# Optimization experiments

Hardware: AMD Instinct MI355X
Metric: run time of the kernel (lower is better)

The kernel has to match this reference:

```python
import jax, jax.numpy as jnp
import numpy as np

B, T, D = 4, 4096, 1024
EPS = 1e-6


def setup_inputs() -> dict:
    key = jax.random.key(0)
    ks = jax.random.split(key, 9)
    s = 0.02  # init scale for weights
    f32 = jnp.float32
    return {
        "x_seq": jax.random.normal(ks[0], (B, T, D), f32),
        "W_q": jax.random.normal(ks[1], (D, D), f32) * s,
        "b_q": jax.random.normal(ks[2], (D,), f32) * s,
        "W_k": jax.random.normal(ks[3], (D, D), f32) * s,
        "b_k": jax.random.normal(ks[4], (D,), f32) * s,
        "W_v": jax.random.normal(ks[5], (D, D), f32) * s,
        "b_v": jax.random.normal(ks[6], (D,), f32) * s,
        "W_a": jax.random.normal(ks[7], (D, D), f32) * s,
        "b_a": jax.random.normal(ks[8], (D,), f32) * s,
    }


def reference(x_seq, W_q, b_q, W_k, b_k, W_v, b_v, W_a, b_a):
    # torch nn.Linear: y = x @ W.T + b
    q = jax.nn.relu(x_seq @ W_q.T + b_q)          # [B,T,D]
    k = jax.nn.relu(x_seq @ W_k.T + b_k)          # [B,T,D]
    v = x_seq @ W_v.T + b_v                        # [B,T,D]
    A = jax.nn.sigmoid(x_seq @ W_a.T + b_a)       # [B,T,D]

    # cumprod_A[b,s,i] = prod_{u>=s} A[b,u,i], via reverse cumsum of logs
    log_g = jax.lax.cumsum(jnp.log(A + 1e-6), axis=1, reverse=True)
    wk = k * jnp.exp(log_g)                        # weighted_k [B,T,D]

    # num[b,t,j] = q_t . S_t[:,j] with S_t = cumsum_{s<=t} (wk_s outer v_s)
    # == causal-masked (q @ wk^T) @ v  (same math, no [B,T,D,D] blowup)
    scores = jnp.einsum('btd,bsd->bts', q, wk)     # [B,T,T]
    Tn = x_seq.shape[1]
    mask = jnp.tril(jnp.ones((Tn, Tn), bool))
    scores = jnp.where(mask, scores, 0.0)

    num = jnp.einsum('bts,bsd->btd', scores, v)    # [B,T,D]
    denom = scores.sum(-1, keepdims=True) + EPS    # q_t . Z_t, [B,T,1]
    return num / denom
```

## Files before the change

kernel.cpp:

```cpp
#include <hip/hip_runtime.h>

typedef unsigned short u16;
typedef unsigned int u32;

typedef __bf16 bf16x8 __attribute__((ext_vector_type(8)));
typedef float f32x4 __attribute__((ext_vector_type(4)));
typedef u16 u16x8 __attribute__((ext_vector_type(8)));

#define TSEQ 4096
#define DDIM 1024
#define NB 4
#define EPSV 1e-6f
#define CPITCH 136

__device__ __forceinline__ u16 f2b(float f) {
    union { float f; u32 u; } v; v.f = f;
    u32 r = v.u + 0x7FFFu + ((v.u >> 16) & 1u);
    return (u16)(r >> 16);
}
__device__ __forceinline__ float b2f(u16 h) {
    union { u32 u; float f; } v; v.u = ((u32)h) << 16; return v.f;
}
__device__ __forceinline__ u16 f2h(float f) {
    union { _Float16 h; u16 u; } v; v.h = (_Float16)f; return v.u;
}
__device__ __forceinline__ float h2f(u16 u) {
    union { u16 u; _Float16 h; } v; v.u = u; return (float)v.h;
}

__global__ __launch_bounds__(256) void k_prep(
    const float* __restrict__ x,
    const float* __restrict__ wq, const float* __restrict__ wk,
    const float* __restrict__ wv, const float* __restrict__ wa,
    const float* __restrict__ bq, const float* __restrict__ bk,
    const float* __restrict__ bv, const float* __restrict__ ba,
    u16* __restrict__ xw, u16* __restrict__ wcat, float* __restrict__ bcat,
    float* __restrict__ denom) {
    int bid = blockIdx.x, tid = threadIdx.x;
    if (bid < 1024) {
        size_t base = (size_t)bid * 4096 + tid;
#pragma unroll
        for (int k = 0; k < 16; ++k) {
            size_t f4 = base + k * 256;
            float4 f = ((const float4*)x)[f4];
            ushort4 u;
            u.x = f2b(f.x); u.y = f2b(f.y); u.z = f2b(f.z); u.w = f2b(f.w);
            *(ushort4*)(xw + f4 * 4) = u;
        }
    } else if (bid < 1280) {
        size_t base = (size_t)(bid - 1024) * 4096 + tid;
#pragma unroll
        for (int k = 0; k < 16; ++k) {
            size_t f4 = base + k * 256;
            int sel = (int)(f4 >> 18);
            const float* src = (sel == 0) ? wq : (sel == 1) ? wk : (sel == 2) ? wv : wa;
            float4 f = ((const float4*)src)[f4 & 262143];
            ushort4 u;
            u.x = f2b(f.x); u.y = f2b(f.y); u.z = f2b(f.z); u.w = f2b(f.w);
            *(ushort4*)(wcat + f4 * 4) = u;
        }
    } else if (bid == 1280) {
#pragma unroll
        for (int c = 0; c < 16; ++c) {
            int j = c * 256 + tid;
            int sel = j >> 10;
            const float* src = (sel == 0) ? bq : (sel == 1) ? bk : (sel == 2) ? bv : ba;
            bcat[j] = src[j & 1023];
        }
    } else {
        float4 z = {0.f, 0.f, 0.f, 0.f};
#pragma unroll
        for (int k = 0; k < 16; ++k)
            ((float4*)denom)[k * 256 + tid] = z;
    }
}

__device__ __forceinline__ void stage_k(u16* __restrict__ dst, const char* __restrict__ base,
                                        int ld2, int kbyte, int wid, int lane) {
#pragma unroll
    for (int c = 0; c < 4; ++c) {
        const char* g = base + c * 8 * ld2 + kbyte;
        char* l = (char*)dst + (wid * 32 + c * 8) * 128 + lane * 16;
        __builtin_amdgcn_global_load_lds((const __attribute__((address_space(1))) u32*)g,
                                         (__attribute__((address_space(3))) u32*)l, 16, 0, 0);
    }
}

__device__ __forceinline__ void mma_tile(const u16* __restrict__ As, const u16* __restrict__ Bs,
                                         f32x4 acc[4][4], int wm, int wn, int quad, int l15) {
#pragma unroll
    for (int kk = 0; kk < 64; kk += 32) {
        int cg = (kk >> 3) + quad;
        bf16x8 a[4], b[4];
#pragma unroll
        for (int i = 0; i < 4; ++i) {
            int arow = wm * 64 + i * 16 + l15;
            int brow = wn * 64 + i * 16 + l15;
            a[i] = *(const bf16x8*)(As + arow * 64 + ((cg ^ (arow & 7)) << 3));
            b[i] = *(const bf16x8*)(Bs + brow * 64 + ((cg ^ (brow & 7)) << 3));
        }
#pragma unroll
        for (int i = 0; i < 4; ++i)
#pragma unroll
            for (int j = 0; j < 4; ++j)
                acc[i][j] = __builtin_amdgcn_mfma_f32_16x16x32_bf16(a[i], b[j], acc[i][j], 0, 0, 0);
    }
}

__global__ __launch_bounds__(256) void k_gemm_qkva(
    const u16* __restrict__ xw, const u16* __restrict__ wcat, const float* __restrict__ bcat,
    u16* __restrict__ qb, u16* __restrict__ kb, u16* __restrict__ vT, u16* __restrict__ gA,
    float* __restrict__ part) {
    __shared__ __align__(16) char smem[CPITCH * 128 * 2];
    u16* As = (u16*)smem;
    u16* Bs = (u16*)(smem + 16384);
    int tid = threadIdx.x;
    int m0 = blockIdx.x * 128, n0 = blockIdx.y * 128;
    int wid = tid >> 6, lane = tid & 63;
    int wm = wid >> 1, wn = wid & 1, quad = lane >> 4, l15 = lane & 15;
    int hxor = (lane & 7) ^ (lane >> 3);
    const char* baA = (const char*)xw + (size_t)(m0 + wid * 32 + (lane >> 3)) * 2048 + hxor * 16;
    const char* baB = (const char*)wcat + (size_t)(n0 + wid * 32 + (lane >> 3)) * 2048 + hxor * 16;
    f32x4 acc[4][4] = {};
#pragma unroll
    for (int k0 = 0; k0 < DDIM; k0 += 64) {
        stage_k(As, baA, 2048, k0 * 2, wid, lane);
        stage_k(Bs, baB, 2048, k0 * 2, wid, lane);
        __syncthreads();
        mma_tile(As, Bs, acc, wm, wn, quad, l15);
        __syncthreads();
    }
    int blk = n0 >> 10, nf0 = n0 & 1023;
    if (blk < 3) {
        u16* Cs = (u16*)smem;
#pragma unroll
        for (int im = 0; im < 4; ++im)
#pragma unroll
        for (int jn = 0; jn < 4; ++jn) {
            float bias = bcat[n0 + wn * 64 + jn * 16 + l15];
#pragma unroll
            for (int r = 0; r < 4; ++r) {
                float z = acc[im][jn][r] + bias;
                if (blk < 2) z = fmaxf(z, 0.f);
                Cs[(wm * 64 + im * 16 + quad * 4 + r) * CPITCH + wn * 64 + jn * 16 + l15] = f2b(z);
            }
        }
        __syncthreads();
        if (blk < 2) {
            u16* dst = (blk == 0) ? qb : kb;
            int r = tid >> 1, ch = (tid & 1) * 64;
            size_t rowo = (size_t)(m0 + r) * DDIM + nf0 + ch;
#pragma unroll
            for (int i = 0; i < 8; ++i)
                *(u16x8*)(dst + rowo + i * 8) = *(const u16x8*)(Cs + r * CPITCH + ch + i * 8);
        } else {
            int j = tid >> 1, th = (tid & 1) * 64;
            int bB = m0 >> 12, t0m = m0 & 4095;
            size_t rowo = (((size_t)(bB * DDIM + nf0 + j)) << 12) + t0m + th;
#pragma unroll
            for (int i = 0; i < 8; ++i) {
                u16x8 vv;
#pragma unroll
                for (int e = 0; e < 8; ++e)
                    vv[e] = Cs[(th + i * 8 + e) * CPITCH + j];
                *(u16x8*)(vT + rowo + i * 8) = vv;
            }
        }
    } else {
        int bB = m0 >> 12;
        int cbase = (m0 & 4095) >> 6;
#pragma unroll
        for (int jn = 0; jn < 4; ++jn) {
            int n = n0 + wn * 64 + jn * 16 + l15;
            float bias = bcat[n];
            int nf = n & 1023;
            float csum = 0.f;
#pragma unroll
            for (int im = 0; im < 4; ++im)
#pragma unroll
            for (int r = 0; r < 4; ++r) {
                int m = m0 + wm * 64 + im * 16 + quad * 4 + r;
                float z = acc[im][jn][r] + bias;
                float g = __logf(1.f / (1.f + __expf(-z)) + 1e-6f);
                gA[(size_t)m * DDIM + nf] = f2h(g);
                csum += g;
            }
            csum += __shfl_xor(csum, 16, 64);
            csum += __shfl_xor(csum, 32, 64);
            if (quad == 0)
                part[((size_t)(bB * 64 + cbase + wm) << 10) + nf] = csum;
        }
    }
}

__global__ __launch_bounds__(256) void k_scan_apply(
    const u16* __restrict__ gA, const float* __restrict__ part, u16* __restrict__ kb) {
    int c = blockIdx.x, b = blockIdx.y;
    int col = blockIdx.z * 256 + threadIdx.x;
    float r = 0.f;
    for (int c2 = c + 1; c2 < 64; ++c2)
        r += part[((size_t)(b * 64 + c2) << 10) + col];
    size_t base = (((size_t)(b * TSEQ + c * 64)) << 10) + col;
#pragma unroll 4
    for (int s = 63; s >= 0; --s) {
        size_t ro = base + ((size_t)s << 10);
        r += h2f(gA[ro]);
        kb[ro] = f2b(b2f(kb[ro]) * __expf(r));
    }
}

__global__ __launch_bounds__(256) void k_scores(
    const u16* __restrict__ qb, const u16* __restrict__ wkb,
    u16* __restrict__ scores, float* __restrict__ denom) {
    int bid = blockIdx.x, b = blockIdx.y;
    int xc = bid & 7, idx = bid >> 3;
    int rs0 = xc, rs1 = 15 - xc, rs2 = 16 + xc, rs3 = 31 - xc;
    int si = 0, rem = idx;
    for (; si < 32; ++si) {
        int n = (rs0 >= si) + (rs1 >= si) + (rs2 >= si) + (rs3 >= si);
        if (rem < n) break;
        rem -= n;
    }
    int ti = rs3, cnt = 0;
    if (rs0 >= si) { if (cnt == rem) ti = rs0; ++cnt; }
    if (rs1 >= si) { if (cnt == rem) ti = rs1; ++cnt; }
    if (rs2 >= si) { if (cnt == rem) ti = rs2; ++cnt; }
    if (rs3 >= si) { if (cnt == rem) ti = rs3; ++cnt; }
    __shared__ __align__(16) char smem[CPITCH * 128 * 2];
    u16* As = (u16*)smem;
    u16* Bs = (u16*)(smem + 16384);
    int tid = threadIdx.x;
    const u16* A = qb + ((size_t)b << 22);
    const u16* Bm = wkb + ((size_t)b << 22);
    int t0 = ti * 128, s0 = si * 128;
    int wid = tid >> 6, lane = tid & 63;
    int wm = wid >> 1, wn = wid & 1, quad = lane >> 4, l15 = lane & 15;
    int hxor = (lane & 7) ^ (lane >> 3);
    const char* baA = (const char*)A + (size_t)(t0 + wid * 32 + (lane >> 3)) * 2048 + hxor * 16;
    const char* baB = (const char*)Bm + (size_t)(s0 + wid * 32 + (lane >> 3)) * 2048 + hxor * 16;
    f32x4 acc[4][4] = {};
#pragma unroll
    for (int k0 = 0; k0 < DDIM; k0 += 64) {
        stage_k(As, baA, 2048, k0 * 2, wid, lane);
        stage_k(Bs, baB, 2048, k0 * 2, wid, lane);
        __syncthreads();
        mma_tile(As, Bs, acc, wm, wn, quad, l15);
        __syncthreads();
    }
    u16* Cs = (u16*)smem;
#pragma unroll
    for (int im = 0; im < 4; ++im) {
#pragma unroll
        for (int r = 0; r < 4; ++r) {
            int trow = t0 + wm * 64 + im * 16 + quad * 4 + r;
            float rs = 0.f;
#pragma unroll
            for (int jn = 0; jn < 4; ++jn) {
                int s = s0 + wn * 64 + jn * 16 + l15;
                float val = acc[im][jn][r];
                if (s > trow) val = 0.f;
                rs += val;
                Cs[(wm * 64 + im * 16 + quad * 4 + r) * CPITCH + wn * 64 + jn * 16 + l15] = f2b(val);
            }
#pragma unroll
            for (int m = 1; m < 16; m <<= 1) rs += __shfl_xor(rs, m, 64);
            if (l15 == 0) atomicAdd(denom + (b << 12) + trow, rs);
        }
    }
    __syncthreads();
    int r = tid >> 1, ch = (tid & 1) * 64;
    size_t rowo = ((size_t)(b * TSEQ + t0 + r) << 12) + s0 + ch;
#pragma unroll
    for (int i = 0; i < 8; ++i)
        *(u16x8*)(scores + rowo + i * 8) = *(const u16x8*)(Cs + r * CPITCH + ch + i * 8);
}

__global__ __launch_bounds__(256) void k_num(
    const u16* __restrict__ scores, const u16* __restrict__ vT,
    const float* __restrict__ denom, float* __restrict__ out) {
    int ji = blockIdx.x, ti = 31 - blockIdx.y, b = blockIdx.z;
    __shared__ __align__(16) u16 As[128 * 64];
    __shared__ __align__(16) u16 Bs[128 * 64];
    int tid = threadIdx.x;
    const u16* A = scores + ((size_t)b << 24);
    const u16* Bm = vT + ((size_t)b << 22);
    int t0 = ti * 128, j0 = ji * 128;
    int wid = tid >> 6, lane = tid & 63;
    int wm = wid >> 1, wn = wid & 1, quad = lane >> 4, l15 = lane & 15;
    int hxor = (lane & 7) ^ (lane >> 3);
    const char* pA = (const char*)A + (size_t)(t0 + wid * 32 + (lane >> 3)) * 8192 + hxor * 16;
    const char* pB = (const char*)Bm + (size_t)(j0 + wid * 32 + (lane >> 3)) * 8192 + hxor * 16;
    f32x4 acc[4][4] = {};
    int kmax = (ti + 1) * 128;
    for (int k0 = 0; k0 < kmax; k0 += 128) {
        stage_k(As, pA, 8192, 0, wid, lane);
        stage_k(Bs, pB, 8192, 0, wid, lane);
        __syncthreads();
        mma_tile(As, Bs, acc, wm, wn, quad, l15);
        __syncthreads();
        stage_k(As, pA, 8192, 128, wid, lane);
        stage_k(Bs, pB, 8192, 128, wid, lane);
        __syncthreads();
        mma_tile(As, Bs, acc, wm, wn, quad, l15);
        __syncthreads();
        pA += 256; pB += 256;
    }
#pragma unroll
    for (int im = 0; im < 4; ++im) {
#pragma unroll
        for (int r = 0; r < 4; ++r) {
            int t = t0 + wm * 64 + im * 16 + quad * 4 + r;
            float den = denom[(b << 12) + t] + EPSV;
#pragma unroll
            for (int jn = 0; jn < 4; ++jn) {
                int j = j0 + wn * 64 + jn * 16 + l15;
                out[((size_t)(b * TSEQ + t) << 10) + j] = acc[im][jn][r] / den;
            }
        }
    }
}

static const size_t OFF_Q      = 0;
static const size_t OFF_WK     = 33554432;
static const size_t OFF_VT     = 67108864;
static const size_t OFF_DENOM  = 100663296;
static const size_t OFF_BCAT   = 100728832;
static const size_t OFF_XW     = 100745216;
static const size_t OFF_WCAT   = 134299648;
static const size_t OFF_GA     = 176242688;
static const size_t OFF_PART   = 243351552;
static const size_t OFF_SCORES = OFF_XW;

extern "C" void kernel_launch(void* const* d_in, const int* in_sizes, int n_in,
                              void* d_out, int out_size, void* d_ws, size_t ws_size,
                              hipStream_t stream) {
    const float* x  = (const float*)d_in[0];
    const float* Wq = (const float*)d_in[1];
    const float* bq = (const float*)d_in[2];
    const float* Wk = (const float*)d_in[3];
    const float* bk = (const float*)d_in[4];
    const float* Wv = (const float*)d_in[5];
    const float* bv = (const float*)d_in[6];
    const float* Wa = (const float*)d_in[7];
    const float* ba = (const float*)d_in[8];
    float* out = (float*)d_out;

    char* W = (char*)d_ws;
    u16* qb      = (u16*)(W + OFF_Q);
    u16* wkb     = (u16*)(W + OFF_WK);
    u16* vT      = (u16*)(W + OFF_VT);
    float* denom = (float*)(W + OFF_DENOM);
    float* bcat  = (float*)(W + OFF_BCAT);
    u16* xw      = (u16*)(W + OFF_XW);
    u16* wcat    = (u16*)(W + OFF_WCAT);
    u16* gA      = (u16*)(W + OFF_GA);
    float* part  = (float*)(W + OFF_PART);
    u16* scores  = (u16*)(W + OFF_SCORES);

    k_prep<<<1282, 256, 0, stream>>>(x, Wq, Wk, Wv, Wa, bq, bk, bv, ba, xw, wcat, bcat, denom);

    k_gemm_qkva<<<dim3(128, 32), 256, 0, stream>>>(xw, wcat, bcat, qb, wkb, vT, gA, part);

    k_scan_apply<<<dim3(64, NB, 4), 256, 0, stream>>>(gA, part, wkb);

    k_scores<<<dim3(528, NB), 256, 0, stream>>>(qb, wkb, scores, denom);

    k_num<<<dim3(8, 32, NB), 256, 0, stream>>>(scores, vT, denom, out);
}
```

Measured before the change: 551.0 us.

## Rewrite QKVA projection GEMM as 256x256 tile with async LDS double-buffered pipeline

The fused projection GEMM moves from 128x128 tiles with 4 waves to 256x256 tiles with 8 waves. Operands are streamed with global_load_lds direct-to-LDS loads into a double buffer, and each k-step is split into four sub-phases with s_setprio, so loads for later k-steps overlap MFMA work. The epilogue now stages the gA output through LDS for coalesced stores instead of scattered 2-byte writes. This uses 128KB of LDS and many more accumulator registers per thread, which caps occupancy, and the hand-written waitcnt and barrier schedule makes correctness depend on exact counting of outstanding loads.

```diff
diff --git a/kernel.cpp b/kernel.cpp
--- a/kernel.cpp
+++ b/kernel.cpp
@@ -12,6 +12,7 @@
 #define NB 4
 #define EPSV 1e-6f
 #define CPITCH 136
+#define EPITCH 264
 
 __device__ __forceinline__ u16 f2b(float f) {
     union { float f; u32 u; } v; v.f = f;
@@ -107,88 +108,166 @@
     }
 }
 
-__global__ __launch_bounds__(256) void k_gemm_qkva(
+#define STG_A(d, h, t) do { \
+    const char* _g = gAp + ((h) * 262144 + wid * 32768 + (t) * 128); \
+    char* _l = lA + ((d) * 32768 + (h) * 16384); \
+    __builtin_amdgcn_global_load_lds((const __attribute__((address_space(1))) u32*)_g, \
+        (__attribute__((address_space(3))) u32*)_l, 16, 0, 0); \
+    __builtin_amdgcn_global_load_lds((const __attribute__((address_space(1))) u32*)(_g + 16384), \
+        (__attribute__((address_space(3))) u32*)(_l + 1024), 16, 0, 0); \
+  } while (0)
+
+#define STG_B(d, h, t) do { \
+    const char* _g = gBp + ((h) * 262144 + wid * 32768 + (t) * 128); \
+    char* _l = lB + ((d) * 32768 + (h) * 16384); \
+    __builtin_amdgcn_global_load_lds((const __attribute__((address_space(1))) u32*)_g, \
+        (__attribute__((address_space(3))) u32*)_l, 16, 0, 0); \
+    __builtin_amdgcn_global_load_lds((const __attribute__((address_space(1))) u32*)(_g + 16384), \
+        (__attribute__((address_space(3))) u32*)(_l + 1024), 16, 0, 0); \
+  } while (0)
+
+#define NOP_ ((void)0)
+#define VM4_ asm volatile("s_waitcnt vmcnt(4)" ::: "memory")
+#define VM0_ asm volatile("s_waitcnt vmcnt(0)" ::: "memory")
+
+#define PHASE(d, qa, qb, STAGE_STMT, VM_STMT) do { \
+    const u16* _Ah = As + (d) * 16384 + (qa) * 8192; \
+    const u16* _Bh = Bs + (d) * 16384 + (qb) * 8192; \
+    bf16x8 _a[4][2]; bf16x8 _b[2][2]; \
+    _Pragma("unroll") \
+    for (int _i = 0; _i < 4; ++_i) { \
+      int _ra = wm * 64 + _i * 16 + l15; \
+      const u16* _p = _Ah + _ra * 64; \
+      _a[_i][0] = *(const bf16x8*)(_p + ((quad ^ (_ra & 7)) << 3)); \
+      _a[_i][1] = *(const bf16x8*)(_p + (((quad + 4) ^ (_ra & 7)) << 3)); \
+    } \
+    _Pragma("unroll") \
+    for (int _j = 0; _j < 2; ++_j) { \
+      int _rb = wn * 32 + _j * 16 + l15; \
+      const u16* _p = _Bh + _rb * 64; \
+      _b[_j][0] = *(const bf16x8*)(_p + ((quad ^ (_rb & 7)) << 3)); \
+      _b[_j][1] = *(const bf16x8*)(_p + (((quad + 4) ^ (_rb & 7)) << 3)); \
+    } \
+    STAGE_STMT; \
+    __builtin_amdgcn_s_barrier(); \
+    asm volatile("s_waitcnt lgkmcnt(0)" ::: "memory"); \
+    __builtin_amdgcn_s_setprio(1); \
+    _Pragma("unroll") \
+    for (int _kk = 0; _kk < 2; ++_kk) \
+      _Pragma("unroll") \
+      for (int _i = 0; _i < 4; ++_i) \
+        _Pragma("unroll") \
+        for (int _j = 0; _j < 2; ++_j) \
+          acc[(qa) * 4 + _i][(qb) * 2 + _j] = __builtin_amdgcn_mfma_f32_16x16x32_bf16( \
+              _a[_i][_kk], _b[_j][_kk], acc[(qa) * 4 + _i][(qb) * 2 + _j], 0, 0, 0); \
+    __builtin_amdgcn_s_setprio(0); \
+    VM_STMT; \
+    __builtin_amdgcn_s_barrier(); \
+  } while (0)
+
+__global__ __launch_bounds__(512, 2) void k_gemm_qkva(
     const u16* __restrict__ xw, const u16* __restrict__ wcat, const float* __restrict__ bcat,
     u16* __restrict__ qb, u16* __restrict__ kb, u16* __restrict__ vT, u16* __restrict__ gA,
     float* __restrict__ part) {
-    __shared__ __align__(16) char smem[CPITCH * 128 * 2];
+    __shared__ __align__(16) char smem[131072];
     u16* As = (u16*)smem;
-    u16* Bs = (u16*)(smem + 16384);
+    u16* Bs = (u16*)(smem + 65536);
     int tid = threadIdx.x;
-    int m0 = blockIdx.x * 128, n0 = blockIdx.y * 128;
     int wid = tid >> 6, lane = tid & 63;
-    int wm = wid >> 1, wn = wid & 1, quad = lane >> 4, l15 = lane & 15;
-    int hxor = (lane & 7) ^ (lane >> 3);
-    const char* baA = (const char*)xw + (size_t)(m0 + wid * 32 + (lane >> 3)) * 2048 + hxor * 16;
-    const char* baB = (const char*)wcat + (size_t)(n0 + wid * 32 + (lane >> 3)) * 2048 + hxor * 16;
-    f32x4 acc[4][4] = {};
-#pragma unroll
-    for (int k0 = 0; k0 < DDIM; k0 += 64) {
-        stage_k(As, baA, 2048, k0 * 2, wid, lane);
-        stage_k(Bs, baB, 2048, k0 * 2, wid, lane);
-        __syncthreads();
-        mma_tile(As, Bs, acc, wm, wn, quad, l15);
-        __syncthreads();
-    }
-    int blk = n0 >> 10, nf0 = n0 & 1023;
-    if (blk < 3) {
-        u16* Cs = (u16*)smem;
-#pragma unroll
-        for (int im = 0; im < 4; ++im)
-#pragma unroll
-        for (int jn = 0; jn < 4; ++jn) {
-            float bias = bcat[n0 + wn * 64 + jn * 16 + l15];
-#pragma unroll
-            for (int r = 0; r < 4; ++r) {
-                float z = acc[im][jn][r] + bias;
-                if (blk < 2) z = fmaxf(z, 0.f);
-                Cs[(wm * 64 + im * 16 + quad * 4 + r) * CPITCH + wn * 64 + jn * 16 + l15] = f2b(z);
+    int wm = wid >> 2, wn = wid & 3;
+    int quad = lane >> 4, l15 = lane & 15;
+    int g8 = lane >> 3, hx = (lane & 7) ^ g8;
+    size_t m0 = (size_t)blockIdx.x * 256, n0 = (size_t)blockIdx.y * 256;
+    const char* gAp = (const char*)xw + (m0 + g8) * 2048 + hx * 16;
+    const char* gBp = (const char*)wcat + (n0 + g8) * 2048 + hx * 16;
+    char* lA = smem + wid * 2048 + lane * 16;
+    char* lB = smem + 65536 + wid * 2048 + lane * 16;
+
+    f32x4 acc[8][4] = {};
+    STG_A(0, 0, 0); STG_A(0, 1, 0);
+    STG_B(0, 0, 0); STG_B(0, 1, 0);
+    STG_A(1, 0, 1); STG_B(1, 0, 1);
+    VM4_;
+    __builtin_amdgcn_s_barrier();
+
+#pragma unroll 2
+    for (int t = 0; t < 14; ++t) {
+        int d = t & 1, dn = d ^ 1;
+        PHASE(d, 0, 0, STG_A(dn, 1, t + 1), NOP_);
+        PHASE(d, 0, 1, STG_B(dn, 1, t + 1), NOP_);
+        PHASE(d, 1, 0, STG_A(d, 0, t + 2), NOP_);
+        PHASE(d, 1, 1, STG_B(d, 0, t + 2), VM4_);
+    }
+    PHASE(0, 0, 0, STG_A(1, 1, 15), NOP_);
+    PHASE(0, 0, 1, STG_B(1, 1, 15), NOP_);
+    PHASE(0, 1, 0, NOP_, NOP_);
+    PHASE(0, 1, 1, NOP_, VM0_);
+    PHASE(1, 0, 0, NOP_, NOP_);
+    PHASE(1, 0, 1, NOP_, NOP_);
+    PHASE(1, 1, 0, NOP_, NOP_);
+    PHASE(1, 1, 1, NOP_, NOP_);
+
+    int blk = (int)(n0 >> 10), nf0 = (int)(n0 & 1023);
+    int bB = (int)(m0 >> 12), t0m = (int)(m0 & 4095);
+    float bias[4];
+#pragma unroll
+    for (int j = 0; j < 4; ++j)
+        bias[j] = bcat[n0 + (size_t)((j >> 1) * 128 + wn * 32 + (j & 1) * 16 + l15)];
+    u16* Cs = (u16*)smem;
+
+#pragma unroll
+    for (int h = 0; h < 2; ++h) {
+        if (h) __syncthreads();
+#pragma unroll
+        for (int j = 0; j < 4; ++j) {
+            float cs = 0.f;
+            int col = (j >> 1) * 128 + wn * 32 + (j & 1) * 16 + l15;
+#pragma unroll
+            for (int i4 = 0; i4 < 4; ++i4) {
+#pragma unroll
+                for (int r = 0; r < 4; ++r) {
+                    float z = acc[h * 4 + i4][j][r] + bias[j];
+                    u16 o;
+                    if (blk < 2) {
+                        o = f2b(fmaxf(z, 0.f));
+                    } else if (blk == 2) {
+                        o = f2b(z);
+                    } else {
+                        float gg = __logf(1.f / (1.f + __expf(-z)) + 1e-6f);
+                        o = f2h(gg);
+                        cs += gg;
+                    }
+                    Cs[(wm * 64 + i4 * 16 + quad * 4 + r) * EPITCH + col] = o;
+                }
             }
-        }
-        __syncthreads();
-        if (blk < 2) {
-            u16* dst = (blk == 0) ? qb : kb;
-            int r = tid >> 1, ch = (tid & 1) * 64;
-            size_t rowo = (size_t)(m0 + r) * DDIM + nf0 + ch;
+            if (blk == 3) {
+                cs += __shfl_xor(cs, 16, 64);
+                cs += __shfl_xor(cs, 32, 64);
+                if (quad == 0) {
+                    int chunk = (t0m >> 6) + h * 2 + wm;
+                    part[((size_t)(bB * 64 + chunk) << 10) + nf0 + col] = cs;
+                }
+            }
+        }
+        __syncthreads();
+        if (blk != 2) {
+            u16* dst = (blk == 0) ? qb : (blk == 1) ? kb : gA;
+            int lr = tid >> 2, c0 = (tid & 3) * 64;
+            size_t rowo = (size_t)(m0 + h * 128 + lr) * 1024 + nf0 + c0;
 #pragma unroll
             for (int i = 0; i < 8; ++i)
-                *(u16x8*)(dst + rowo + i * 8) = *(const u16x8*)(Cs + r * CPITCH + ch + i * 8);
+                *(u16x8*)(dst + rowo + i * 8) = *(const u16x8*)(Cs + lr * EPITCH + c0 + i * 8);
         } else {
-            int j = tid >> 1, th = (tid & 1) * 64;
-            int bB = m0 >> 12, t0m = m0 & 4095;
-            size_t rowo = (((size_t)(bB * DDIM + nf0 + j)) << 12) + t0m + th;
+            int jc = tid >> 1, th = (tid & 1) * 64;
+            size_t rowo = (((size_t)(bB * 1024 + nf0 + jc)) << 12) + t0m + h * 128 + th;
 #pragma unroll
             for (int i = 0; i < 8; ++i) {
                 u16x8 vv;
 #pragma unroll
                 for (int e = 0; e < 8; ++e)
-                    vv[e] = Cs[(th + i * 8 + e) * CPITCH + j];
+                    vv[e] = Cs[(th + i * 8 + e) * EPITCH + jc];
                 *(u16x8*)(vT + rowo + i * 8) = vv;
             }
-        }
-    } else {
-        int bB = m0 >> 12;
-        int cbase = (m0 & 4095) >> 6;
-#pragma unroll
-        for (int jn = 0; jn < 4; ++jn) {
-            int n = n0 + wn * 64 + jn * 16 + l15;
-            float bias = bcat[n];
-            int nf = n & 1023;
-            float csum = 0.f;
-#pragma unroll
-            for (int im = 0; im < 4; ++im)
-#pragma unroll
-            for (int r = 0; r < 4; ++r) {
-                int m = m0 + wm * 64 + im * 16 + quad * 4 + r;
-                float z = acc[im][jn][r] + bias;
-                float g = __logf(1.f / (1.f + __expf(-z)) + 1e-6f);
-                gA[(size_t)m * DDIM + nf] = f2h(g);
-                csum += g;
-            }
-            csum += __shfl_xor(csum, 16, 64);
-            csum += __shfl_xor(csum, 32, 64);
-            if (quad == 0)
-                part[((size_t)(bB * 64 + cbase + wm) << 10) + nf] = csum;
         }
     }
 }
@@ -359,7 +438,7 @@
 
     k_prep<<<1282, 256, 0, stream>>>(x, Wq, Wk, Wv, Wa, bq, bk, bv, ba, xw, wcat, bcat, denom);
 
-    k_gemm_qkva<<<dim3(128, 32), 256, 0, stream>>>(xw, wcat, bcat, qb, wkb, vT, gA, part);
+    k_gemm_qkva<<<dim3(64, 16), 512, 0, stream>>>(xw, wcat, bcat, qb, wkb, vT, gA, part);
 
     k_scan_apply<<<dim3(64, NB, 4), 256, 0, stream>>>(gA, part, wkb);
 
```

Measured after the change: 559.4 us. Within noise of the previous version (+1.5%).
